# Kernel tuning notes

Measured on AMD Instinct MI355X. Metric: run time of the kernel, lower is better.

## Reference

```python
import jax, jax.numpy as jnp
import numpy as np

N_USERS = 16384
N_ITEMS = 8192
DIM = 64
AVG_DEG = 64          # average implicit-feedback items per user
U_MEAN = 0.05         # self.u = data.float().mean(); constant buffer, not a parameter


def setup_inputs() -> dict:
    key = jax.random.key(0)
    k1, k2, k3 = jax.random.split(key, 3)
    Q1 = jax.random.normal(k1, (N_ITEMS, DIM), dtype=jnp.float32) * 0.1
    Q2 = jax.random.normal(k2, (N_ITEMS, DIM), dtype=jnp.float32) * 0.1
    P = jax.random.normal(k3, (N_USERS, DIM), dtype=jnp.float32) * 0.1
    bu = jnp.zeros((N_USERS,), dtype=jnp.float32)
    bi = jnp.zeros((N_ITEMS,), dtype=jnp.float32)

    # Ragged implicit-feedback structure (CSR-style): sorted segment ids per user,
    # with every user guaranteed >= 1 item (len(Ni[u]) > 0 in the original).
    nnz = N_USERS * AVG_DEG
    rng = np.random.default_rng(0)
    extra = rng.integers(0, N_USERS, size=nnz - N_USERS)
    seg_ids = np.sort(np.concatenate([np.arange(N_USERS), extra])).astype(np.int32)
    flat_items = rng.integers(0, N_ITEMS, size=nnz).astype(np.int32)

    return {
        "Q1": Q1, "Q2": Q2, "P": P, "bu": bu, "bi": bi,
        "flat_items": jnp.asarray(flat_items),
        "seg_ids": jnp.asarray(seg_ids),
    }


def reference(Q1, Q2, P, bu, bi, flat_items, seg_ids):
    n_users = P.shape[0]
    # counts[u] = len(Ni[u]); Ysum[u] = Q2[Ni[u]].sum(0)  (fused ragged segment reduce)
    counts = jax.ops.segment_sum(
        jnp.ones_like(seg_ids, dtype=Q2.dtype), seg_ids, num_segments=n_users)
    Ysum = jax.ops.segment_sum(Q2[flat_items], seg_ids, num_segments=n_users)
    P_full = Ysum / jnp.sqrt(counts)[:, None] + P          # [U, D]

    # b = bu[:,None] + bi[None,:]; user_id=None path: b[[None]] adds a leading dim.
    scores = jnp.einsum('ud,id->ui', P_full, Q1) + bu[:, None] + bi[None, :] + U_MEAN
    return (jax.nn.sigmoid(scores) * 5.0)[None]           # [1, U, I]
```

## Files before the change

### kernel.cpp

```cpp
#include <hip/hip_runtime.h>

#define U_CNT 16384
#define I_CNT 8192
#define DIM 64
#define BAND 16
#define CHUNK 256
#define NSTEP 32
#define LDS_STRIDE 68
#define NEG_LOG2E (-1.4426950408889634f)

typedef __bf16 bf16x8 __attribute__((ext_vector_type(8)));
typedef float f32x4 __attribute__((ext_vector_type(4)));

__device__ __forceinline__ unsigned short f32_to_bf16_rtn(float f) {
    unsigned int b = __float_as_uint(f);
    b += 0x7fffu + ((b >> 16) & 1u);
    return (unsigned short)(b >> 16);
}

__global__ __launch_bounds__(256) void prep_kernel(
    const float* __restrict__ Q1, unsigned short* __restrict__ Q1bf,
    const int* __restrict__ segs, int nnz, int* __restrict__ bounds)
{
    if (blockIdx.x < 2048) {
        int i = blockIdx.x * 256 + threadIdx.x;
        Q1bf[i] = f32_to_bf16_rtn(Q1[i]);
    } else {
        int i = (blockIdx.x - 2048) * 256 + threadIdx.x;
        if (i >= nnz) return;
        if (i == 0) bounds[segs[0]] = 0;
        else if (segs[i] != segs[i - 1]) bounds[segs[i]] = i;
        if (i == nnz - 1) bounds[U_CNT] = nnz;
    }
}

__global__ __launch_bounds__(256) void pfull_kernel(
    const float* __restrict__ Q2, const float* __restrict__ P,
    const int* __restrict__ items, const int* __restrict__ bounds,
    unsigned short* __restrict__ Pbf)
{
    int u = (blockIdx.x * 256 + threadIdx.x) >> 6;
    int lane = threadIdx.x & 63;
    if (u >= U_CNT) return;
    int start = bounds[u];
    int end   = bounds[u + 1];

    float s = 0.f;
    int j = start;
    for (; j + 3 < end; j += 4) {
        int i0 = items[j], i1 = items[j + 1], i2 = items[j + 2], i3 = items[j + 3];
        float v0 = Q2[i0 * DIM + lane];
        float v1 = Q2[i1 * DIM + lane];
        float v2 = Q2[i2 * DIM + lane];
        float v3 = Q2[i3 * DIM + lane];
        s += (v0 + v1) + (v2 + v3);
    }
    for (; j < end; ++j) s += Q2[items[j] * DIM + lane];

    int cnt = end - start;
    float val = s * rsqrtf((float)cnt) + P[u * DIM + lane];
    Pbf[u * DIM + lane] = f32_to_bf16_rtn(val);
}

__global__ __launch_bounds__(256) void gemm_sig_kernel(
    const unsigned short* __restrict__ Abf, const unsigned short* __restrict__ Bbf,
    const float* __restrict__ bu, const float* __restrict__ bi,
    float* __restrict__ out)
{
    const int lane = threadIdx.x & 63;
    const int wid  = threadIdx.x >> 6;
    const int r = lane & 15, g = lane >> 4;
    const int member = blockIdx.x & 31;
    const int group  = blockIdx.x >> 5;
    const int col0 = member * CHUNK + wid * 64;

    __shared__ float lds_all[4][BAND * LDS_STRIDE];
    float* lds = lds_all[wid];

    bf16x8 b[4][2];
    float bi_f[4];
#pragma unroll
    for (int nf = 0; nf < 4; ++nf) {
        bi_f[nf] = bi[col0 + nf * 16 + r] + 0.05f;
#pragma unroll
        for (int ks = 0; ks < 2; ++ks)
            b[nf][ks] = *reinterpret_cast<const bf16x8*>(
                &Bbf[(col0 + nf * 16 + r) * DIM + ks * 32 + g * 8]);
    }

    for (int s = 0; s < NSTEP; ++s) {
        const int band = (group + s * 32) * BAND;

        bf16x8 a[2];
#pragma unroll
        for (int ks = 0; ks < 2; ++ks)
            a[ks] = *reinterpret_cast<const bf16x8*>(
                &Abf[(band + r) * DIM + ks * 32 + g * 8]);

        float bu_g[4];
#pragma unroll
        for (int j = 0; j < 4; ++j) bu_g[j] = bu[band + g * 4 + j];

        f32x4 acc[4] = {};
#pragma unroll
        for (int ks = 0; ks < 2; ++ks)
#pragma unroll
            for (int nf = 0; nf < 4; ++nf)
                acc[nf] = __builtin_amdgcn_mfma_f32_16x16x32_bf16(
                    a[ks], b[nf][ks], acc[nf], 0, 0, 0);

#pragma unroll
        for (int nf = 0; nf < 4; ++nf)
#pragma unroll
            for (int j = 0; j < 4; ++j) {
                float x = (acc[nf][j] + bu_g[j] + bi_f[nf]) * NEG_LOG2E;
                float e = __builtin_amdgcn_exp2f(x);
                float v = 5.f * __builtin_amdgcn_rcpf(1.f + e);
                lds[(g * 4 + j) * LDS_STRIDE + nf * 16 + r] = v;
            }

#pragma unroll
        for (int i = 0; i < 4; ++i) {
            const int row = i * 4 + g;
            f32x4 v = *reinterpret_cast<const f32x4*>(&lds[row * LDS_STRIDE + r * 4]);
            __builtin_nontemporal_store(v, reinterpret_cast<f32x4*>(
                &out[(size_t)(band + row) * I_CNT + col0 + r * 4]));
        }
    }
}

extern "C" void kernel_launch(void* const* d_in, const int* in_sizes, int n_in,
                              void* d_out, int out_size, void* d_ws, size_t ws_size,
                              hipStream_t stream)
{
    const float* Q1 = (const float*)d_in[0];
    const float* Q2 = (const float*)d_in[1];
    const float* P  = (const float*)d_in[2];
    const float* bu = (const float*)d_in[3];
    const float* bi = (const float*)d_in[4];
    const int* items = (const int*)d_in[5];
    const int* segs  = (const int*)d_in[6];
    const int nnz = in_sizes[5];

    unsigned short* Pbf  = (unsigned short*)d_ws;
    unsigned short* Q1bf = Pbf + U_CNT * DIM;
    int* bounds = (int*)(Q1bf + I_CNT * DIM);

    int boundsBlocks = (nnz + 255) / 256;
    prep_kernel<<<2048 + boundsBlocks, 256, 0, stream>>>(Q1, Q1bf, segs, nnz, bounds);
    pfull_kernel<<<U_CNT / 4, 256, 0, stream>>>(Q2, P, items, bounds, Pbf);
    gemm_sig_kernel<<<32 * 32, 256, 0, stream>>>(Pbf, Q1bf, bu, bi, (float*)d_out);
}
```

Baseline: 130.6 us.

## Drop prep kernel: binary-search segment bounds and convert Q1 to bf16 in GEMM

Removes the separate prep kernel. Segment start and end are now found by per-user binary search over the sorted seg_ids inside the P_full kernel. Q1 is converted from fp32 to bf16 on the fly when the GEMM kernel loads its B fragments. This saves one launch and the Q1bf and bounds round trips through memory. In exchange, every wavefront runs two serial binary searches of about 20 dependent loads each, and each GEMM block reads fp32 Q1, which is twice the bytes.

Measured after the change: 153.0 us. +17.2%, slower.

```diff
diff --git a/kernel.cpp b/kernel.cpp
--- a/kernel.cpp
+++ b/kernel.cpp
@@ -11,6 +11,7 @@
 
 typedef __bf16 bf16x8 __attribute__((ext_vector_type(8)));
 typedef float f32x4 __attribute__((ext_vector_type(4)));
+typedef short short8 __attribute__((ext_vector_type(8)));
 
 __device__ __forceinline__ unsigned short f32_to_bf16_rtn(float f) {
     unsigned int b = __float_as_uint(f);
@@ -18,32 +19,21 @@
     return (unsigned short)(b >> 16);
 }
 
-__global__ __launch_bounds__(256) void prep_kernel(
-    const float* __restrict__ Q1, unsigned short* __restrict__ Q1bf,
-    const int* __restrict__ segs, int nnz, int* __restrict__ bounds)
-{
-    if (blockIdx.x < 2048) {
-        int i = blockIdx.x * 256 + threadIdx.x;
-        Q1bf[i] = f32_to_bf16_rtn(Q1[i]);
-    } else {
-        int i = (blockIdx.x - 2048) * 256 + threadIdx.x;
-        if (i >= nnz) return;
-        if (i == 0) bounds[segs[0]] = 0;
-        else if (segs[i] != segs[i - 1]) bounds[segs[i]] = i;
-        if (i == nnz - 1) bounds[U_CNT] = nnz;
-    }
-}
-
 __global__ __launch_bounds__(256) void pfull_kernel(
     const float* __restrict__ Q2, const float* __restrict__ P,
-    const int* __restrict__ items, const int* __restrict__ bounds,
-    unsigned short* __restrict__ Pbf)
+    const int* __restrict__ items, const int* __restrict__ segs,
+    int nnz, unsigned short* __restrict__ Pbf)
 {
     int u = (blockIdx.x * 256 + threadIdx.x) >> 6;
     int lane = threadIdx.x & 63;
     if (u >= U_CNT) return;
-    int start = bounds[u];
-    int end   = bounds[u + 1];
+
+    int lo = 0, hi = nnz;
+    while (lo < hi) { int m = (lo + hi) >> 1; if (segs[m] < u) lo = m + 1; else hi = m; }
+    int start = lo;
+    hi = nnz;
+    while (lo < hi) { int m = (lo + hi) >> 1; if (segs[m] <= u) lo = m + 1; else hi = m; }
+    int end = lo;
 
     float s = 0.f;
     int j = start;
@@ -63,7 +53,7 @@
 }
 
 __global__ __launch_bounds__(256) void gemm_sig_kernel(
-    const unsigned short* __restrict__ Abf, const unsigned short* __restrict__ Bbf,
+    const unsigned short* __restrict__ Abf, const float* __restrict__ Q1,
     const float* __restrict__ bu, const float* __restrict__ bi,
     float* __restrict__ out)
 {
@@ -83,9 +73,18 @@
     for (int nf = 0; nf < 4; ++nf) {
         bi_f[nf] = bi[col0 + nf * 16 + r] + 0.05f;
 #pragma unroll
-        for (int ks = 0; ks < 2; ++ks)
-            b[nf][ks] = *reinterpret_cast<const bf16x8*>(
-                &Bbf[(col0 + nf * 16 + r) * DIM + ks * 32 + g * 8]);
+        for (int ks = 0; ks < 2; ++ks) {
+            const float* src = &Q1[(col0 + nf * 16 + r) * DIM + ks * 32 + g * 8];
+            f32x4 vlo = *reinterpret_cast<const f32x4*>(src);
+            f32x4 vhi = *reinterpret_cast<const f32x4*>(src + 4);
+            short8 t;
+#pragma unroll
+            for (int e = 0; e < 4; ++e) {
+                t[e]     = (short)f32_to_bf16_rtn(vlo[e]);
+                t[e + 4] = (short)f32_to_bf16_rtn(vhi[e]);
+            }
+            b[nf][ks] = *reinterpret_cast<bf16x8*>(&t);
+        }
     }
 
     for (int s = 0; s < NSTEP; ++s) {
@@ -142,12 +141,8 @@
     const int* segs  = (const int*)d_in[6];
     const int nnz = in_sizes[5];
 
-    unsigned short* Pbf  = (unsigned short*)d_ws;
-    unsigned short* Q1bf = Pbf + U_CNT * DIM;
-    int* bounds = (int*)(Q1bf + I_CNT * DIM);
+    unsigned short* Pbf = (unsigned short*)d_ws;
 
-    int boundsBlocks = (nnz + 255) / 256;
-    prep_kernel<<<2048 + boundsBlocks, 256, 0, stream>>>(Q1, Q1bf, segs, nnz, bounds);
-    pfull_kernel<<<U_CNT / 4, 256, 0, stream>>>(Q2, P, items, bounds, Pbf);
-    gemm_sig_kernel<<<32 * 32, 256, 0, stream>>>(Pbf, Q1bf, bu, bi, (float*)d_out);
+    pfull_kernel<<<U_CNT / 4, 256, 0, stream>>>(Q2, P, items, segs, nnz, Pbf);
+    gemm_sig_kernel<<<32 * 32, 256, 0, stream>>>(Pbf, Q1, bu, bi, (float*)d_out);
 }
```
